# Optimization experiments

Hardware: AMD Instinct MI355X
Metric: run time of the kernel (lower is better)

## Reference

```python
import jax, jax.numpy as jnp
import numpy as np

N, D = 8192, 4096  # D must be a power of 2 for FWHT


def fwht(x):
    """Unnormalized Fast Walsh-Hadamard Transform along the last axis (len = 2^k)."""
    orig_shape = x.shape
    d = orig_shape[-1]
    x = x.reshape(-1, d)
    h = 1
    while h < d:
        x = x.reshape(-1, d // (2 * h), 2, h)
        a = x[..., 0, :]
        b = x[..., 1, :]
        x = jnp.stack([a + b, a - b], axis=-2)
        h *= 2
    return x.reshape(orig_shape)


def setup_inputs() -> dict:
    key = jax.random.key(0)
    k = jax.random.split(key, 6)
    return {
        "x": jax.random.normal(k[0], (N, D), dtype=jnp.float32),
        "s1": jax.random.normal(k[1], (D,), dtype=jnp.float32),
        "s2": jax.random.normal(k[2], (D,), dtype=jnp.float32),
        "g_mu": jax.random.normal(k[3], (D,), dtype=jnp.float32),
        "g_rho": jax.random.normal(k[4], (D,), dtype=jnpp.float32) if False else jax.random.normal(k[4], (D,), dtype=jnp.float32),
        "epsilon": jax.random.normal(k[5], (D,), dtype=jnp.float32),
    }


def reference(x, s1, s2, g_mu, g_rho, epsilon):
    # W(u) = diag(s1) H diag(u) H diag(s2); forward (sample=True):
    #   b = x @ W(g_mu).T + x @ W(softplus(g_rho) * epsilon).T
    # Per-row (H symmetric): x @ W(u).T = s1 * fwht(u * fwht(s2 * x)).
    t = fwht(x * s2)                                  # [N, D], shared between both terms
    g_noise = jax.nn.softplus(g_rho) * epsilon        # g_sigma_sqrt @ epsilon
    b = s1 * fwht(t * g_mu) + s1 * fwht(t * g_noise)  # [N, D]
    return b
```

## Files before the change

kernel.cpp:

```cpp
#include <hip/hip_runtime.h>
#include <math.h>

#define D 4096
#define RPB 2
#define STRIDE 68

typedef float f4 __attribute__((ext_vector_type(4)));

__device__ __forceinline__ void wave_lds_fence() {
    __asm__ volatile("s_waitcnt lgkmcnt(0)" ::: "memory");
}

__device__ __forceinline__ void fwht64(float* v) {
#pragma unroll
    for (int h = 1; h < 64; h <<= 1) {
#pragma unroll
        for (int i = 0; i < 64; i += 2 * h) {
#pragma unroll
            for (int j = i; j < i + h; ++j) {
                const float a = v[j];
                const float b = v[j + h];
                v[j]     = a + b;
                v[j + h] = a - b;
            }
        }
    }
}

__global__ void whvi_prep(const float* __restrict__ g_mu,
                          const float* __restrict__ g_rho,
                          const float* __restrict__ eps,
                          float* __restrict__ gq) {
    const int i = blockIdx.x * 256 + threadIdx.x;
    const int l = i >> 6, k = i & 63;
    const int e = (l & 3) | (k << 2) | ((l >> 2) << 8);
    const float r  = g_rho[e];
    const float sp = (r > 20.f) ? r : log1pf(expf(r));
    gq[i] = g_mu[e] + sp * eps[e];
}

__global__ void __launch_bounds__(128, 4) whvi_main(
    const float* __restrict__ x,  const float* __restrict__ s1,
    const float* __restrict__ s2, const float* __restrict__ gq,
    const float* __restrict__ g_mu, const float* __restrict__ g_rho,
    const float* __restrict__ eps, float* __restrict__ out) {
    __shared__ alignas(16) float lds_all[RPB][64 * STRIDE];
    const int l = threadIdx.x & 63;
    const int w = threadIdx.x >> 6;
    float* lds = lds_all[w];
    const long long row = (long long)blockIdx.x * RPB + w;
    const float* xr = x + row * (long long)D;
    float v[64];

#pragma unroll
    for (int q = 0; q < 16; ++q)
        *reinterpret_cast<f4*>(&v[4 * q]) =
            *reinterpret_cast<const f4*>(xr + (l << 2) + (q << 8));

#pragma unroll
    for (int q = 0; q < 16; ++q) {
        const f4 s = *reinterpret_cast<const f4*>(s2 + (l << 2) + (q << 8));
        v[4 * q + 0] *= s.x;
        v[4 * q + 1] *= s.y;
        v[4 * q + 2] *= s.z;
        v[4 * q + 3] *= s.w;
    }

    fwht64(v);

#pragma unroll
    for (int r = 0; r < 64; ++r)
        lds[r * STRIDE + l] = v[r];
    wave_lds_fence();
#pragma unroll
    for (int t = 0; t < 16; ++t)
        *reinterpret_cast<f4*>(&v[4 * t]) =
            *reinterpret_cast<const f4*>(&lds[l * STRIDE + 4 * t]);

    fwht64(v);

    if (gq) {
#pragma unroll
        for (int t = 0; t < 16; ++t) {
            const f4 g = *reinterpret_cast<const f4*>(gq + (l << 6) + (t << 2));
            v[4 * t + 0] *= g.x;
            v[4 * t + 1] *= g.y;
            v[4 * t + 2] *= g.z;
            v[4 * t + 3] *= g.w;
        }
    } else {
#pragma unroll
        for (int k = 0; k < 64; ++k) {
            const int e = (l & 3) | (k << 2) | ((l >> 2) << 8);
            const float r  = g_rho[e];
            const float sp = (r > 20.f) ? r : log1pf(expf(r));
            v[k] *= g_mu[e] + sp * eps[e];
        }
    }

    fwht64(v);

    wave_lds_fence();
#pragma unroll
    for (int t = 0; t < 16; ++t)
        *reinterpret_cast<f4*>(&lds[l * STRIDE + 4 * t]) =
            *reinterpret_cast<const f4*>(&v[4 * t]);
    wave_lds_fence();
#pragma unroll
    for (int r = 0; r < 64; ++r)
        v[r] = lds[r * STRIDE + l];

    fwht64(v);

    float* outr = out + row * (long long)D;
#pragma unroll
    for (int q = 0; q < 16; ++q) {
        const f4 s = *reinterpret_cast<const f4*>(s1 + (l << 2) + (q << 8));
        f4 o;
        o.x = v[4 * q + 0] * s.x;
        o.y = v[4 * q + 1] * s.y;
        o.z = v[4 * q + 2] * s.z;
        o.w = v[4 * q + 3] * s.w;
        *reinterpret_cast<f4*>(outr + (l << 2) + (q << 8)) = o;
    }
}

extern "C" void kernel_launch(void* const* d_in, const int* in_sizes, int n_in,
                              void* d_out, int out_size, void* d_ws, size_t ws_size,
                              hipStream_t stream) {
    const float* x     = (const float*)d_in[0];
    const float* s1    = (const float*)d_in[1];
    const float* s2    = (const float*)d_in[2];
    const float* g_mu  = (const float*)d_in[3];
    const float* g_rho = (const float*)d_in[4];
    const float* eps   = (const float*)d_in[5];
    float* out = (float*)d_out;
    const int rows = in_sizes[0] / D;

    float* gq = nullptr;
    if (ws_size >= (size_t)D * sizeof(float)) {
        gq = (float*)d_ws;
        whvi_prep<<<D / 256, 256, 0, stream>>>(g_mu, g_rho, eps, gq);
    }
    whvi_main<<<rows / RPB, 128, 0, stream>>>(x, s1, s2, gq, g_mu, g_rho, eps, out);
}
```

Measured before the change: 254.9 us.

## Double-buffer row loads into LDS with async global_load_lds across persistent rows

Each single-wave block now processes 8 rows in sequence, prefetching the next row directly into a double-buffered LDS slot with global_load_lds while computing the current one. The padded LDS transpose is replaced by an XOR-swizzled layout that reuses the staging buffer, and the fallback path for the noise vector is removed, so the workspace is now assumed. The aim is to hide global load latency behind the FWHT compute. In exchange the grid has fewer, smaller blocks, and it relies on vmcnt counting to order the async loads, which may cost occupancy or risk incorrect waits.

```diff
diff --git a/kernel.cpp b/kernel.cpp
--- a/kernel.cpp
+++ b/kernel.cpp
@@ -1,14 +1,30 @@
 #include <hip/hip_runtime.h>
 #include <math.h>
+#include <stdint.h>
 
 #define D 4096
-#define RPB 2
-#define STRIDE 68
+#define ROWS 8
 
 typedef float f4 __attribute__((ext_vector_type(4)));
 
-__device__ __forceinline__ void wave_lds_fence() {
+__device__ __forceinline__ void lds_fence() {
     __asm__ volatile("s_waitcnt lgkmcnt(0)" ::: "memory");
+}
+__device__ __forceinline__ void wait_vm16() {
+    __asm__ volatile("s_waitcnt vmcnt(16)" ::: "memory");
+}
+__device__ __forceinline__ void wait_vm0() {
+    __asm__ volatile("s_waitcnt vmcnt(0)" ::: "memory");
+}
+
+__device__ __forceinline__ void async_row_load(const float* gsrc, float* ldsdst, int l) {
+#pragma unroll
+    for (int q = 0; q < 16; ++q) {
+        __builtin_amdgcn_global_load_lds(
+            (const __attribute__((address_space(1))) void*)(gsrc + q * 256 + 4 * l),
+            (__attribute__((address_space(3))) void*)(ldsdst + q * 256),
+            16, 0, 0);
+    }
 }
 
 __device__ __forceinline__ void fwht64(float* v) {
@@ -39,89 +55,91 @@
     gq[i] = g_mu[e] + sp * eps[e];
 }
 
-__global__ void __launch_bounds__(128, 4) whvi_main(
+__global__ void __launch_bounds__(64) whvi_main(
     const float* __restrict__ x,  const float* __restrict__ s1,
     const float* __restrict__ s2, const float* __restrict__ gq,
     const float* __restrict__ g_mu, const float* __restrict__ g_rho,
     const float* __restrict__ eps, float* __restrict__ out) {
-    __shared__ alignas(16) float lds_all[RPB][64 * STRIDE];
-    const int l = threadIdx.x & 63;
-    const int w = threadIdx.x >> 6;
-    float* lds = lds_all[w];
-    const long long row = (long long)blockIdx.x * RPB + w;
-    const float* xr = x + row * (long long)D;
+    __shared__ alignas(16) float B[2][D];
+    const int l = threadIdx.x;
+    const long long r0 = (long long)blockIdx.x * ROWS;
+    const float* xbase = x + r0 * (long long)D;
     float v[64];
 
-#pragma unroll
-    for (int q = 0; q < 16; ++q)
-        *reinterpret_cast<f4*>(&v[4 * q]) =
-            *reinterpret_cast<const f4*>(xr + (l << 2) + (q << 8));
+    async_row_load(xbase, B[0], l);
+    wait_vm0();
+
+    for (int i = 0; i < ROWS; ++i) {
+        float* cur = B[i & 1];
+        float* nxt = B[(i + 1) & 1];
+
+        if (i) wait_vm16();
+
+        if (i + 1 < ROWS)
+            async_row_load(xbase + (long long)(i + 1) * D, nxt, l);
 
 #pragma unroll
-    for (int q = 0; q < 16; ++q) {
-        const f4 s = *reinterpret_cast<const f4*>(s2 + (l << 2) + (q << 8));
-        v[4 * q + 0] *= s.x;
-        v[4 * q + 1] *= s.y;
-        v[4 * q + 2] *= s.z;
-        v[4 * q + 3] *= s.w;
-    }
-
-    fwht64(v);
+        for (int q = 0; q < 16; ++q)
+            *reinterpret_cast<f4*>(&v[4 * q]) =
+                *reinterpret_cast<const f4*>(cur + q * 256 + 4 * l);
 
 #pragma unroll
-    for (int r = 0; r < 64; ++r)
-        lds[r * STRIDE + l] = v[r];
-    wave_lds_fence();
+        for (int q = 0; q < 16; ++q) {
+            const f4 s = *reinterpret_cast<const f4*>(s2 + q * 256 + 4 * l);
+            v[4 * q + 0] *= s.x;
+            v[4 * q + 1] *= s.y;
+            v[4 * q + 2] *= s.z;
+            v[4 * q + 3] *= s.w;
+        }
+
+        fwht64(v);
+
+        lds_fence();
 #pragma unroll
-    for (int t = 0; t < 16; ++t)
-        *reinterpret_cast<f4*>(&v[4 * t]) =
-            *reinterpret_cast<const f4*>(&lds[l * STRIDE + 4 * t]);
+        for (int r = 0; r < 64; ++r)
+            cur[r * 64 + (l ^ (r & 28))] = v[r];
+        lds_fence();
+#pragma unroll
+        for (int t = 0; t < 16; ++t)
+            *reinterpret_cast<f4*>(&v[4 * t]) =
+                *reinterpret_cast<const f4*>(cur + l * 64 + ((4 * t) ^ (l & 28)));
 
-    fwht64(v);
+        fwht64(v);
 
-    if (gq) {
 #pragma unroll
         for (int t = 0; t < 16; ++t) {
-            const f4 g = *reinterpret_cast<const f4*>(gq + (l << 6) + (t << 2));
+            const f4 g = *reinterpret_cast<const f4*>(gq + (l << 6) + 4 * t);
             v[4 * t + 0] *= g.x;
             v[4 * t + 1] *= g.y;
             v[4 * t + 2] *= g.z;
             v[4 * t + 3] *= g.w;
         }
-    } else {
+
+        fwht64(v);
+
+        lds_fence();
 #pragma unroll
-        for (int k = 0; k < 64; ++k) {
-            const int e = (l & 3) | (k << 2) | ((l >> 2) << 8);
-            const float r  = g_rho[e];
-            const float sp = (r > 20.f) ? r : log1pf(expf(r));
-            v[k] *= g_mu[e] + sp * eps[e];
+        for (int t = 0; t < 16; ++t)
+            *reinterpret_cast<f4*>(cur + l * 64 + ((4 * t) ^ (l & 28))) =
+                *reinterpret_cast<const f4*>(&v[4 * t]);
+        lds_fence();
+#pragma unroll
+        for (int r = 0; r < 64; ++r)
+            v[r] = cur[r * 64 + (l ^ (r & 28))];
+
+        fwht64(v);
+
+        float* outr = out + (r0 + i) * (long long)D;
+#pragma unroll
+        for (int q = 0; q < 16; ++q) {
+            const f4 s = *reinterpret_cast<const f4*>(s1 + q * 256 + 4 * l);
+            f4 o;
+            o.x = v[4 * q + 0] * s.x;
+            o.y = v[4 * q + 1] * s.y;
+            o.z = v[4 * q + 2] * s.z;
+            o.w = v[4 * q + 3] * s.w;
+            *reinterpret_cast<f4*>(outr + q * 256 + 4 * l) = o;
         }
-    }
-
-    fwht64(v);
-
-    wave_lds_fence();
-#pragma unroll
-    for (int t = 0; t < 16; ++t)
-        *reinterpret_cast<f4*>(&lds[l * STRIDE + 4 * t]) =
-            *reinterpret_cast<const f4*>(&v[4 * t]);
-    wave_lds_fence();
-#pragma unroll
-    for (int r = 0; r < 64; ++r)
-        v[r] = lds[r * STRIDE + l];
-
-    fwht64(v);
-
-    float* outr = out + row * (long long)D;
-#pragma unroll
-    for (int q = 0; q < 16; ++q) {
-        const f4 s = *reinterpret_cast<const f4*>(s1 + (l << 2) + (q << 8));
-        f4 o;
-        o.x = v[4 * q + 0] * s.x;
-        o.y = v[4 * q + 1] * s.y;
-        o.z = v[4 * q + 2] * s.z;
-        o.w = v[4 * q + 3] * s.w;
-        *reinterpret_cast<f4*>(outr + (l << 2) + (q << 8)) = o;
     }
 }
 
@@ -137,10 +155,7 @@
     float* out = (float*)d_out;
     const int rows = in_sizes[0] / D;
 
-    float* gq = nullptr;
-    if (ws_size >= (size_t)D * sizeof(float)) {
-        gq = (float*)d_ws;
-        whvi_prep<<<D / 256, 256, 0, stream>>>(g_mu, g_rho, eps, gq);
-    }
-    whvi_main<<<rows / RPB, 128, 0, stream>>>(x, s1, s2, gq, g_mu, g_rho, eps, out);
+    float* gq = (float*)d_ws;
+    whvi_prep<<<D / 256, 256, 0, stream>>>(g_mu, g_rho, eps, gq);
+    whvi_main<<<rows / ROWS, 64, 0, stream>>>(x, s1, s2, gq, g_mu, g_rho, eps, out);
 }
```

After: 276.6 us. 8.5% more time.
